# Kernel optimization log

Hardware: AMD Instinct MI355X
Metric: run time of the kernel (lower is better)

The kernel has to match this reference:

```python
import jax, jax.numpy as jnp
import numpy as np

N_NODES = 100000
N_EDGES = 1600000
D_IN = 128
HIDDEN = 128
N_CLASS = 10
N_LAYERS = 3


def setup_inputs() -> dict:
    key = jax.random.key(0)
    ks = jax.random.split(key, 12)
    x = jax.random.normal(ks[0], (N_NODES, D_IN), dtype=jnp.float32)
    edge_index = jax.random.randint(ks[1], (2, N_EDGES), 0, N_NODES, dtype=jnp.int64)
    edge_weight = jax.random.uniform(ks[2], (N_EDGES,), dtype=jnp.float32)
    # Per-layer GIN MLP params. D_IN == HIDDEN so all 3 layers stack cleanly.
    s = 1.0 / np.sqrt(HIDDEN)
    Wa = jax.random.uniform(ks[3], (N_LAYERS, HIDDEN, HIDDEN), minval=-s, maxval=s, dtype=jnp.float32)
    ba = jax.random.uniform(ks[4], (N_LAYERS, HIDDEN), minval=-s, maxval=s, dtype=jnp.float32)
    Wb = jax.random.uniform(ks[5], (N_LAYERS, HIDDEN, HIDDEN), minval=-s, maxval=s, dtype=jnp.float32)
    bb = jax.random.uniform(ks[6], (N_LAYERS, HIDDEN), minval=-s, maxval=s, dtype=jnp.float32)
    fcW = jax.random.uniform(ks[7], (HIDDEN, N_CLASS), minval=-s, maxval=s, dtype=jnp.float32)
    fcb = jax.random.uniform(ks[8], (N_CLASS,), minval=-s, maxval=s, dtype=jnp.float32)
    return {"x": x, "edge_index": edge_index, "edge_weight": edge_weight,
            "Wa": Wa, "ba": ba, "Wb": Wb, "bb": bb, "fcW": fcW, "fcb": fcb}


def reference(x, edge_index, edge_weight, Wa, ba, Wb, bb, fcW, fcb):
    # NOTE: edge_weight is loaded in the original forward but never used
    # (GINConv is invoked with only (x, edge_index)); we faithfully ignore it.
    src = edge_index[0]
    dst = edge_index[1]
    h = x
    for i in range(N_LAYERS):
        # GIN aggregation: (1 + eps) * h + sum_{j in N(i)} h_j, with eps = 0
        agg = jax.ops.segment_sum(h[src], dst, num_segments=N_NODES)  # [N, H]
        z = h + agg
        # 2-layer MLP: Linear -> ELU -> Linear -> ELU
        z = jax.nn.elu(z @ Wa[i] + ba[i])
        h = jax.nn.elu(z @ Wb[i] + bb[i])
    return h @ fcW + fcb  # [N, n_class]
```

## Files before the change

kernel.cpp:

```cpp
#include <hip/hip_runtime.h>
#include <hip/hip_bf16.h>
#include <math.h>

#define N_NODES 100000
#define N_PAD 100032
#define N_EDGES 1600000
#define HID 128
#define N_CLASS 10

#define NR2 256
#define RANGE2 391
#define PCAP2 8192
#define P_BLOCKS 512
#define P_SLICE (N_EDGES / P_BLOCKS)

typedef float f32x4 __attribute__((ext_vector_type(4)));
typedef short short8 __attribute__((ext_vector_type(8)));
typedef unsigned short us4 __attribute__((ext_vector_type(4)));

__device__ __forceinline__ unsigned short f2bf(float x) {
    unsigned u = __float_as_uint(x);
    unsigned r = u + 0x7FFF + ((u >> 16) & 1);
    return (unsigned short)(r >> 16);
}
__device__ __forceinline__ float bf2f(unsigned short h) {
    return __uint_as_float(((unsigned)h) << 16);
}
__device__ __forceinline__ float elu(float x) {
    return x > 0.f ? x : (expf(x) - 1.f);
}
__device__ __forceinline__ float4 us4f(us4 v) {
    float4 o;
    o.x = bf2f(v.x); o.y = bf2f(v.y); o.z = bf2f(v.z); o.w = bf2f(v.w);
    return o;
}


__global__ __launch_bounds__(256) void part_k(const int* __restrict__ src,
                                              const int* __restrict__ dst,
                                              int* __restrict__ gcnt,
                                              unsigned* __restrict__ gbuf) {
    __shared__ unsigned stash[P_SLICE];
    __shared__ unsigned char rbuf[P_SLICE];
    __shared__ int hist[NR2], cur[NR2], base[NR2];
    hist[threadIdx.x] = 0;
    cur[threadIdx.x] = 0;
    __syncthreads();
    const int e0 = blockIdx.x * P_SLICE;
    for (int i = threadIdx.x; i < P_SLICE; i += 256) {
        unsigned s = (unsigned)src[e0 + i];
        unsigned d = (unsigned)dst[e0 + i];
        unsigned r = d / RANGE2;
        unsigned dloc = d - r * RANGE2;
        stash[i] = s | (dloc << 17);
        rbuf[i] = (unsigned char)r;
        atomicAdd(&hist[r], 1);
    }
    __syncthreads();
    base[threadIdx.x] = atomicAdd(&gcnt[threadIdx.x], hist[threadIdx.x]);
    __syncthreads();
    for (int i = threadIdx.x; i < P_SLICE; i += 256) {
        unsigned r = rbuf[i];
        int off = atomicAdd(&cur[r], 1);
        int pos = base[r] + off;
        if (pos < PCAP2) gbuf[(size_t)r * PCAP2 + pos] = stash[i];
    }
}

__global__ void scanc_k(const int* __restrict__ gcnt, int* __restrict__ colbase,
                        int* __restrict__ row_ptr) {
    __shared__ int sh[NR2];
    int v = gcnt[threadIdx.x];
    sh[threadIdx.x] = v;
    __syncthreads();
    for (int off = 1; off < NR2; off <<= 1) {
        int t = (threadIdx.x >= off) ? sh[threadIdx.x - off] : 0;
        __syncthreads();
        sh[threadIdx.x] += t;
        __syncthreads();
    }
    colbase[threadIdx.x] = sh[threadIdx.x] - v;
    if (threadIdx.x == 0) row_ptr[N_NODES] = N_EDGES;
}

__global__ __launch_bounds__(256) void csort_k(const unsigned* __restrict__ gbuf,
                                               const int* __restrict__ gcnt,
                                               const int* __restrict__ colbase,
                                               int* __restrict__ row_ptr,
                                               int* __restrict__ col) {
    __shared__ int sorted[PCAP2];
    __shared__ int hist[512];
    __shared__ int cnt[512];
    __shared__ int run[400];
    const int q = blockIdx.x;
    const int tid = threadIdx.x;
    const int n2 = gcnt[q];
    const int cb = colbase[q];
    const int node0 = q * RANGE2;
    const unsigned* buf = gbuf + (size_t)q * PCAP2;

    hist[tid] = 0; hist[tid + 256] = 0;
    __syncthreads();
    for (int i = tid; i < n2; i += 256)
        atomicAdd(&hist[buf[i] >> 17], 1);
    __syncthreads();
    cnt[tid] = hist[tid];
    cnt[tid + 256] = hist[tid + 256];
    __syncthreads();
    for (int off = 1; off < 512; off <<= 1) {
        int v0 = (tid >= off) ? hist[tid - off] : 0;
        int v1 = hist[tid + 256 - off];
        __syncthreads();
        hist[tid] += v0;
        hist[tid + 256] += v1;
        __syncthreads();
    }
#pragma unroll
    for (int b = 0; b < 2; b++) {
        int i = tid + 256 * b;
        if (i < RANGE2) {
            int excl = hist[i] - cnt[i];
            run[i] = excl;
            int node = node0 + i;
            if (node < N_NODES) row_ptr[node] = cb + excl;
        }
    }
    __syncthreads();
    for (int i = tid; i < n2; i += 256) {
        unsigned w = buf[i];
        int pos = atomicAdd(&run[w >> 17], 1);
        sorted[pos] = (int)(w & 0x1FFFF);
    }
    __syncthreads();
    for (int i = tid; i < n2; i += 256) col[cb + i] = sorted[i];
}

__global__ __launch_bounds__(256) void cast_k(const float* __restrict__ x,
                                              unsigned short* __restrict__ hb) {
    int i = blockIdx.x * blockDim.x + threadIdx.x;
    if (i < N_NODES * (HID / 4)) {
        float4 v = ((const float4*)x)[i];
        us4 o = {f2bf(v.x), f2bf(v.y), f2bf(v.z), f2bf(v.w)};
        ((us4*)hb)[i] = o;
    }
}

__global__ void wsplit_k(const float* __restrict__ Wa, const float* __restrict__ Wb,
                         unsigned short* __restrict__ Whp) {
    int f = blockIdx.x * blockDim.x + threadIdx.x;
    if (f >= 6 * 16384) return;
    int g = f >> 14;
    int r = f & 16383;
    int j = r & 7;
    int L = (r >> 3) & 63;
    int t = r >> 9;
    int kb = t >> 3, nt = t & 7;
    int k = kb * 32 + ((L >> 4) & 3) * 8 + j;
    int n = nt * 16 + (L & 15);
    int layer = g >> 1;
    const float* W = (g & 1) ? Wb : Wa;
    Whp[f] = f2bf(W[layer * 16384 + k * 128 + n]);
}

__global__ void fcsplit_k(const float* __restrict__ fcW,
                          unsigned short* __restrict__ fcWph) {
    int f = blockIdx.x * blockDim.x + threadIdx.x;
    if (f >= 2048) return;
    int j = f & 7;
    int L = (f >> 3) & 63;
    int kb = f >> 9;
    int k = kb * 32 + ((L >> 4) & 3) * 8 + j;
    int n = L & 15;
    fcWph[f] = f2bf((n < N_CLASS) ? fcW[k * N_CLASS + n] : 0.f);
}

__global__ __launch_bounds__(256) void agg_k(const unsigned short* __restrict__ h,
                                             const int* __restrict__ row_ptr,
                                             const int* __restrict__ col,
                                             float* __restrict__ z) {
    const int half = (blockIdx.x * blockDim.x + threadIdx.x) >> 5;
    const int lane = threadIdx.x & 31;
    const int halfbase = threadIdx.x & 32;
    if (half >= N_NODES) return;
    const us4* hp = (const us4*)h;
    float4 acc = us4f(hp[(size_t)half * 32 + lane]);
    const int beg = row_ptr[half];
    const int end = row_ptr[half + 1];

    for (int base = beg; base < end; base += 32) {
        const int n = min(32, end - base);
        int myidx = (lane < n) ? col[base + lane] : 0;
        int j = 0;
        for (; j + 4 <= n; j += 4) {
            int i0 = __shfl(myidx, halfbase + j + 0, 64);
            int i1 = __shfl(myidx, halfbase + j + 1, 64);
            int i2 = __shfl(myidx, halfbase + j + 2, 64);
            int i3 = __shfl(myidx, halfbase + j + 3, 64);
            float4 v0 = us4f(hp[(size_t)i0 * 32 + lane]);
            float4 v1 = us4f(hp[(size_t)i1 * 32 + lane]);
            float4 v2 = us4f(hp[(size_t)i2 * 32 + lane]);
            float4 v3 = us4f(hp[(size_t)i3 * 32 + lane]);
            acc.x += v0.x; acc.y += v0.y; acc.z += v0.z; acc.w += v0.w;
            acc.x += v1.x; acc.y += v1.y; acc.z += v1.z; acc.w += v1.w;
            acc.x += v2.x; acc.y += v2.y; acc.z += v2.z; acc.w += v2.w;
            acc.x += v3.x; acc.y += v3.y; acc.z += v3.z; acc.w += v3.w;
        }
        for (; j < n; j++) {
            int i0 = __shfl(myidx, halfbase + j, 64);
            float4 v0 = us4f(hp[(size_t)i0 * 32 + lane]);
            acc.x += v0.x; acc.y += v0.y; acc.z += v0.z; acc.w += v0.w;
        }
    }
    ((float4*)z)[(size_t)half * 32 + lane] = acc;
}

__device__ __forceinline__ void gemm_phase(
    const unsigned short* Aph_,
    const unsigned short* __restrict__ Whi_g,
    const float* __restrict__ bias, int tid, f32x4 acc[2][4]) {
    const int L = tid & 63;
    const int w = tid >> 6;
    const int mt0 = (w >> 1) * 2;
    const int nt0 = (w & 1) * 4;
    const int lan15 = L & 15;
#pragma unroll
    for (int n = 0; n < 4; n++) {
        float b = bias[(nt0 + n) * 16 + lan15];
        f32x4 bv = {b, b, b, b};
        acc[0][n] = bv;
        acc[1][n] = bv;
    }
#pragma unroll
    for (int kb = 0; kb < 4; kb++) {
        short8 ah0 = *(const short8*)&Aph_[(((mt0 + 0) * 4 + kb) * 64 + L) * 8];
        short8 ah1 = *(const short8*)&Aph_[(((mt0 + 1) * 4 + kb) * 64 + L) * 8];
#pragma unroll
        for (int n = 0; n < 4; n++) {
            int widx = ((kb * 8 + nt0 + n) * 64 + L) * 8;
            short8 bh = *(const short8*)&Whi_g[widx];
            acc[0][n] = __builtin_amdgcn_mfma_f32_16x16x32_bf16(ah0, bh, acc[0][n], 0, 0, 0);
            acc[1][n] = __builtin_amdgcn_mfma_f32_16x16x32_bf16(ah1, bh, acc[1][n], 0, 0, 0);
        }
    }
}

template <int FC>
__device__ __forceinline__ void mlp_body(
    const float* __restrict__ zin,
    const unsigned short* __restrict__ Wahp,
    const unsigned short* __restrict__ Wbhp,
    const float* __restrict__ ba, const float* __restrict__ bb,
    unsigned short* __restrict__ hout,
    const unsigned short* __restrict__ fcWph,
    const float* __restrict__ fcb, float* __restrict__ out) {
    __shared__ unsigned short Aph[8192];

    const int tid = threadIdx.x;
    const int L = tid & 63;
    const int w = tid >> 6;
    const int mt0 = (w >> 1) * 2;
    const int nt0 = (w & 1) * 4;
    const int lan15 = L & 15;
    const int quad = L >> 4;
    const size_t node_base = (size_t)blockIdx.x * 64;

    {
        const float4* zin4 = (const float4*)(zin + node_base * HID);
#pragma unroll
        for (int r = 0; r < 8; r++) {
            int f = tid + 256 * r;
            int m = f >> 5;
            int k0 = (f & 31) * 4;
            float4 zv = zin4[f];
            int kb = k0 >> 5;
            int q = (k0 & 31) >> 3;
            int j0 = k0 & 7;
            int idx = (((m >> 4) * 4 + kb) * 64 + ((m & 15) + 16 * q)) * 8 + j0;
            us4 h4 = {f2bf(zv.x), f2bf(zv.y), f2bf(zv.z), f2bf(zv.w)};
            *(us4*)&Aph[idx] = h4;
        }
    }
    __syncthreads();

    {
        f32x4 acc[2][4];
        gemm_phase(Aph, Wahp, ba, tid, acc);
        __syncthreads();
#pragma unroll
        for (int i = 0; i < 2; i++) {
#pragma unroll
            for (int n = 0; n < 4; n++) {
                int kdim = (nt0 + n) * 16 + lan15;
                int kb2 = kdim >> 5;
                int q2 = (kdim & 31) >> 3;
                int j2 = kdim & 7;
#pragma unroll
                for (int r = 0; r < 4; r++) {
                    float v = elu(acc[i][n][r]);
                    int mrow = quad * 4 + r;
                    int idx = (((mt0 + i) * 4 + kb2) * 64 + (mrow + 16 * q2)) * 8 + j2;
                    Aph[idx] = f2bf(v);
                }
            }
        }
    }
    __syncthreads();

    {
        f32x4 acc[2][4];
        gemm_phase(Aph, Wbhp, bb, tid, acc);
        if (FC == 0) {
#pragma unroll
            for (int i = 0; i < 2; i++) {
#pragma unroll
                for (int n = 0; n < 4; n++) {
                    int ncol = (nt0 + n) * 16 + lan15;
#pragma unroll
                    for (int r = 0; r < 4; r++) {
                        int mrow = (mt0 + i) * 16 + quad * 4 + r;
                        hout[(node_base + mrow) * HID + ncol] = f2bf(elu(acc[i][n][r]));
                    }
                }
            }
        } else {
            __syncthreads();
#pragma unroll
            for (int i = 0; i < 2; i++) {
#pragma unroll
                for (int n = 0; n < 4; n++) {
                    int kdim = (nt0 + n) * 16 + lan15;
                    int kb2 = kdim >> 5;
                    int q2 = (kdim & 31) >> 3;
                    int j2 = kdim & 7;
#pragma unroll
                    for (int r = 0; r < 4; r++) {
                        float v = elu(acc[i][n][r]);
                        int mrow = quad * 4 + r;
                        int idx = (((mt0 + i) * 4 + kb2) * 64 + (mrow + 16 * q2)) * 8 + j2;
                        Aph[idx] = f2bf(v);
                    }
                }
            }
            __syncthreads();
            if ((w & 1) == 0) {
#pragma unroll
                for (int i = 0; i < 2; i++) {
                    int mt = mt0 + i;
                    float b = (lan15 < N_CLASS) ? fcb[lan15] : 0.f;
                    f32x4 acc2 = {b, b, b, b};
#pragma unroll
                    for (int kb = 0; kb < 4; kb++) {
                        short8 a = *(const short8*)&Aph[((mt * 4 + kb) * 64 + L) * 8];
                        short8 bh = *(const short8*)&fcWph[(kb * 64 + L) * 8];
                        acc2 = __builtin_amdgcn_mfma_f32_16x16x32_bf16(a, bh, acc2, 0, 0, 0);
                    }
#pragma unroll
                    for (int r = 0; r < 4; r++) {
                        size_t node = node_base + mt * 16 + quad * 4 + r;
                        if (node < N_NODES && lan15 < N_CLASS)
                            out[node * N_CLASS + lan15] = acc2[r];
                    }
                }
            }
        }
    }
}

__global__ __launch_bounds__(256) void mlp2_k(
    const float* __restrict__ zin,
    const unsigned short* __restrict__ Wahp,
    const unsigned short* __restrict__ Wbhp,
    const float* __restrict__ ba, const float* __restrict__ bb,
    unsigned short* __restrict__ hout) {
    mlp_body<0>(zin, Wahp, Wbhp, ba, bb, hout, nullptr, nullptr, nullptr);
}

__global__ __launch_bounds__(256) void mlp3_k(
    const float* __restrict__ zin,
    const unsigned short* __restrict__ Wahp,
    const unsigned short* __restrict__ Wbhp,
    const float* __restrict__ ba, const float* __restrict__ bb,
    const unsigned short* __restrict__ fcWph,
    const float* __restrict__ fcb, float* __restrict__ out) {
    mlp_body<1>(zin, Wahp, Wbhp, ba, bb, nullptr, fcWph, fcb, out);
}


extern "C" void kernel_launch(void* const* d_in, const int* in_sizes, int n_in,
                              void* d_out, int out_size, void* d_ws, size_t ws_size,
                              hipStream_t stream) {
    const float* x = (const float*)d_in[0];
    const int* ei = (const int*)d_in[1];
    const float* Wa = (const float*)d_in[3];
    const float* ba = (const float*)d_in[4];
    const float* Wb = (const float*)d_in[5];
    const float* bb = (const float*)d_in[6];
    const float* fcW = (const float*)d_in[7];
    const float* fcb = (const float*)d_in[8];
    float* out = (float*)d_out;

    const int* src = ei;
    const int* dst = ei + N_EDGES;

    char* w = (char*)d_ws;
    float* zbuf = (float*)w;          w += (size_t)N_PAD * HID * 4;
    unsigned short* hb = (unsigned short*)w; w += (size_t)N_PAD * HID * 2;
    int* row_ptr = (int*)w;  w += ((size_t)N_NODES + 8) * 4;
    int* gcnt = (int*)w;     w += NR2 * 4;
    int* colbase = (int*)w;  w += NR2 * 4;
    int* col = (int*)w;      w += (size_t)N_EDGES * 4;
    unsigned short* Whp = (unsigned short*)w; w += 6 * 16384 * 2;
    unsigned short* fcWph = (unsigned short*)w; w += 2048 * 2;
    unsigned* gbuf = (unsigned*)w; w += (size_t)NR2 * PCAP2 * 4;

    wsplit_k<<<(6 * 16384 + 255) / 256, 256, 0, stream>>>(Wa, Wb, Whp);
    fcsplit_k<<<8, 256, 0, stream>>>(fcW, fcWph);
    cast_k<<<(N_NODES * (HID / 4) + 255) / 256, 256, 0, stream>>>(x, hb);

    hipMemsetAsync(gcnt, 0, NR2 * 4, stream);
    part_k<<<P_BLOCKS, 256, 0, stream>>>(src, dst, gcnt, gbuf);
    scanc_k<<<1, 256, 0, stream>>>(gcnt, colbase, row_ptr);
    csort_k<<<NR2, 256, 0, stream>>>(gbuf, gcnt, colbase, row_ptr, col);

    const int AGG_BLOCKS = (N_NODES * 32 + 255) / 256;
    const int MLP_BLOCKS = (N_NODES + 63) / 64;

    agg_k<<<AGG_BLOCKS, 256, 0, stream>>>(hb, row_ptr, col, zbuf);
    mlp2_k<<<MLP_BLOCKS, 256, 0, stream>>>(zbuf, Whp, Whp + 16384, ba, bb, hb);
    agg_k<<<AGG_BLOCKS, 256, 0, stream>>>(hb, row_ptr, col, zbuf);
    mlp2_k<<<MLP_BLOCKS, 256, 0, stream>>>(zbuf, Whp + 2 * 16384, Whp + 3 * 16384,
                                           ba + 128, bb + 128, hb);
    agg_k<<<AGG_BLOCKS, 256, 0, stream>>>(hb, row_ptr, col, zbuf);
    mlp3_k<<<MLP_BLOCKS, 256, 0, stream>>>(zbuf, Whp + 4 * 16384, Whp + 5 * 16384,
                                           ba + 256, bb + 256,
                                           fcWph, fcb, out);
}
```

Measured before the change: 419.4 us.

## Fuse setup kernels, fold column scan into csort, store aggregates as bf16

Merges the partition, cast, weight-split and fc-split kernels into one multi-role setup kernel. The column-base scan moves into each csort block, which removes two launches. The aggregation output is now written as bf16 instead of fp32, and the first MLP GEMM reads A fragments directly from global memory instead of staging through LDS. Together these cut launch count and halve the z-buffer traffic, at the cost of rounding the aggregated sums to bf16 and doing uncoalesced per-lane global A loads.

```diff
diff --git a/kernel.cpp b/kernel.cpp
--- a/kernel.cpp
+++ b/kernel.cpp
@@ -13,6 +13,9 @@
 #define PCAP2 8192
 #define P_BLOCKS 512
 #define P_SLICE (N_EDGES / P_BLOCKS)
+#define CAST_ITEMS (N_NODES * (HID / 4))
+#define CAST_BLOCKS ((CAST_ITEMS + 2047) / 2048)
+#define WSPLIT_BLOCKS 384
 
 typedef float f32x4 __attribute__((ext_vector_type(4)));
 typedef short short8 __attribute__((ext_vector_type(8)));
@@ -35,67 +38,104 @@
     return o;
 }
 
-
-__global__ __launch_bounds__(256) void part_k(const int* __restrict__ src,
-                                              const int* __restrict__ dst,
-                                              int* __restrict__ gcnt,
-                                              unsigned* __restrict__ gbuf) {
+__global__ __launch_bounds__(256) void setup_k(
+    const int* __restrict__ src, const int* __restrict__ dst,
+    int* __restrict__ gcnt, unsigned* __restrict__ gbuf,
+    const float* __restrict__ x, unsigned short* __restrict__ hb,
+    const float* __restrict__ Wa, const float* __restrict__ Wb,
+    unsigned short* __restrict__ Whp,
+    const float* __restrict__ fcW, unsigned short* __restrict__ fcWph,
+    int* __restrict__ row_ptr) {
     __shared__ unsigned stash[P_SLICE];
     __shared__ unsigned char rbuf[P_SLICE];
     __shared__ int hist[NR2], cur[NR2], base[NR2];
-    hist[threadIdx.x] = 0;
-    cur[threadIdx.x] = 0;
-    __syncthreads();
-    const int e0 = blockIdx.x * P_SLICE;
-    for (int i = threadIdx.x; i < P_SLICE; i += 256) {
-        unsigned s = (unsigned)src[e0 + i];
-        unsigned d = (unsigned)dst[e0 + i];
-        unsigned r = d / RANGE2;
-        unsigned dloc = d - r * RANGE2;
-        stash[i] = s | (dloc << 17);
-        rbuf[i] = (unsigned char)r;
-        atomicAdd(&hist[r], 1);
-    }
-    __syncthreads();
-    base[threadIdx.x] = atomicAdd(&gcnt[threadIdx.x], hist[threadIdx.x]);
-    __syncthreads();
-    for (int i = threadIdx.x; i < P_SLICE; i += 256) {
-        unsigned r = rbuf[i];
-        int off = atomicAdd(&cur[r], 1);
-        int pos = base[r] + off;
-        if (pos < PCAP2) gbuf[(size_t)r * PCAP2 + pos] = stash[i];
-    }
-}
-
-__global__ void scanc_k(const int* __restrict__ gcnt, int* __restrict__ colbase,
-                        int* __restrict__ row_ptr) {
-    __shared__ int sh[NR2];
-    int v = gcnt[threadIdx.x];
-    sh[threadIdx.x] = v;
-    __syncthreads();
-    for (int off = 1; off < NR2; off <<= 1) {
-        int t = (threadIdx.x >= off) ? sh[threadIdx.x - off] : 0;
-        __syncthreads();
-        sh[threadIdx.x] += t;
-        __syncthreads();
-    }
-    colbase[threadIdx.x] = sh[threadIdx.x] - v;
-    if (threadIdx.x == 0) row_ptr[N_NODES] = N_EDGES;
+    const int b = blockIdx.x;
+    const int tid = threadIdx.x;
+
+    if (b < P_BLOCKS) {
+        hist[tid] = 0;
+        cur[tid] = 0;
+        __syncthreads();
+        const int e0 = b * P_SLICE;
+        for (int i = tid; i < P_SLICE; i += 256) {
+            unsigned s = (unsigned)src[e0 + i];
+            unsigned d = (unsigned)dst[e0 + i];
+            unsigned r = d / RANGE2;
+            unsigned dloc = d - r * RANGE2;
+            stash[i] = s | (dloc << 17);
+            rbuf[i] = (unsigned char)r;
+            atomicAdd(&hist[r], 1);
+        }
+        __syncthreads();
+        base[tid] = atomicAdd(&gcnt[tid], hist[tid]);
+        __syncthreads();
+        for (int i = tid; i < P_SLICE; i += 256) {
+            unsigned r = rbuf[i];
+            int off = atomicAdd(&cur[r], 1);
+            int pos = base[r] + off;
+            if (pos < PCAP2) gbuf[(size_t)r * PCAP2 + pos] = stash[i];
+        }
+    } else if (b < P_BLOCKS + CAST_BLOCKS) {
+        const int cb = b - P_BLOCKS;
+#pragma unroll
+        for (int it = 0; it < 8; it++) {
+            int i = cb * 2048 + it * 256 + tid;
+            if (i < CAST_ITEMS) {
+                float4 v = ((const float4*)x)[i];
+                us4 o = {f2bf(v.x), f2bf(v.y), f2bf(v.z), f2bf(v.w)};
+                ((us4*)hb)[i] = o;
+            }
+        }
+    } else if (b < P_BLOCKS + CAST_BLOCKS + WSPLIT_BLOCKS) {
+        int f = (b - P_BLOCKS - CAST_BLOCKS) * 256 + tid;
+        int g = f >> 14;
+        int r = f & 16383;
+        int j = r & 7;
+        int L = (r >> 3) & 63;
+        int t = r >> 9;
+        int kb = t >> 3, nt = t & 7;
+        int k = kb * 32 + ((L >> 4) & 3) * 8 + j;
+        int n = nt * 16 + (L & 15);
+        int layer = g >> 1;
+        const float* W = (g & 1) ? Wb : Wa;
+        Whp[f] = f2bf(W[layer * 16384 + k * 128 + n]);
+    } else {
+#pragma unroll
+        for (int it = 0; it < 8; it++) {
+            int f = it * 256 + tid;
+            int j = f & 7;
+            int L = (f >> 3) & 63;
+            int kb = f >> 9;
+            int k = kb * 32 + ((L >> 4) & 3) * 8 + j;
+            int n = L & 15;
+            fcWph[f] = f2bf((n < N_CLASS) ? fcW[k * N_CLASS + n] : 0.f);
+        }
+        if (tid == 0) row_ptr[N_NODES] = N_EDGES;
+    }
 }
 
 __global__ __launch_bounds__(256) void csort_k(const unsigned* __restrict__ gbuf,
                                                const int* __restrict__ gcnt,
-                                               const int* __restrict__ colbase,
                                                int* __restrict__ row_ptr,
                                                int* __restrict__ col) {
     __shared__ int sorted[PCAP2];
     __shared__ int hist[512];
     __shared__ int cnt[512];
     __shared__ int run[400];
+    __shared__ int gsc[NR2];
     const int q = blockIdx.x;
     const int tid = threadIdx.x;
+
+    gsc[tid] = gcnt[tid];
+    __syncthreads();
+    for (int off = 1; off < NR2; off <<= 1) {
+        int t = (tid >= off) ? gsc[tid - off] : 0;
+        __syncthreads();
+        gsc[tid] += t;
+        __syncthreads();
+    }
+    const int cb = (q > 0) ? gsc[q - 1] : 0;
     const int n2 = gcnt[q];
-    const int cb = colbase[q];
     const int node0 = q * RANGE2;
     const unsigned* buf = gbuf + (size_t)q * PCAP2;
 
@@ -116,8 +156,8 @@
         __syncthreads();
     }
 #pragma unroll
-    for (int b = 0; b < 2; b++) {
-        int i = tid + 256 * b;
+    for (int bb = 0; bb < 2; bb++) {
+        int i = tid + 256 * bb;
         if (i < RANGE2) {
             int excl = hist[i] - cnt[i];
             run[i] = excl;
@@ -135,49 +175,10 @@
     for (int i = tid; i < n2; i += 256) col[cb + i] = sorted[i];
 }
 
-__global__ __launch_bounds__(256) void cast_k(const float* __restrict__ x,
-                                              unsigned short* __restrict__ hb) {
-    int i = blockIdx.x * blockDim.x + threadIdx.x;
-    if (i < N_NODES * (HID / 4)) {
-        float4 v = ((const float4*)x)[i];
-        us4 o = {f2bf(v.x), f2bf(v.y), f2bf(v.z), f2bf(v.w)};
-        ((us4*)hb)[i] = o;
-    }
-}
-
-__global__ void wsplit_k(const float* __restrict__ Wa, const float* __restrict__ Wb,
-                         unsigned short* __restrict__ Whp) {
-    int f = blockIdx.x * blockDim.x + threadIdx.x;
-    if (f >= 6 * 16384) return;
-    int g = f >> 14;
-    int r = f & 16383;
-    int j = r & 7;
-    int L = (r >> 3) & 63;
-    int t = r >> 9;
-    int kb = t >> 3, nt = t & 7;
-    int k = kb * 32 + ((L >> 4) & 3) * 8 + j;
-    int n = nt * 16 + (L & 15);
-    int layer = g >> 1;
-    const float* W = (g & 1) ? Wb : Wa;
-    Whp[f] = f2bf(W[layer * 16384 + k * 128 + n]);
-}
-
-__global__ void fcsplit_k(const float* __restrict__ fcW,
-                          unsigned short* __restrict__ fcWph) {
-    int f = blockIdx.x * blockDim.x + threadIdx.x;
-    if (f >= 2048) return;
-    int j = f & 7;
-    int L = (f >> 3) & 63;
-    int kb = f >> 9;
-    int k = kb * 32 + ((L >> 4) & 3) * 8 + j;
-    int n = L & 15;
-    fcWph[f] = f2bf((n < N_CLASS) ? fcW[k * N_CLASS + n] : 0.f);
-}
-
 __global__ __launch_bounds__(256) void agg_k(const unsigned short* __restrict__ h,
                                              const int* __restrict__ row_ptr,
                                              const int* __restrict__ col,
-                                             float* __restrict__ z) {
+                                             unsigned short* __restrict__ z) {
     const int half = (blockIdx.x * blockDim.x + threadIdx.x) >> 5;
     const int lane = threadIdx.x & 31;
     const int halfbase = threadIdx.x & 32;
@@ -211,10 +212,43 @@
             acc.x += v0.x; acc.y += v0.y; acc.z += v0.z; acc.w += v0.w;
         }
     }
-    ((float4*)z)[(size_t)half * 32 + lane] = acc;
-}
-
-__device__ __forceinline__ void gemm_phase(
+    us4 o = {f2bf(acc.x), f2bf(acc.y), f2bf(acc.z), f2bf(acc.w)};
+    ((us4*)z)[(size_t)half * 32 + lane] = o;
+}
+
+__device__ __forceinline__ void gemm1_g(
+    const unsigned short* __restrict__ zrow,
+    const unsigned short* __restrict__ Whi_g,
+    const float* __restrict__ bias, int tid, f32x4 acc[2][4]) {
+    const int L = tid & 63;
+    const int w = tid >> 6;
+    const int mt0 = (w >> 1) * 2;
+    const int nt0 = (w & 1) * 4;
+    const int lan15 = L & 15;
+    const int quad = L >> 4;
+#pragma unroll
+    for (int n = 0; n < 4; n++) {
+        float b = bias[(nt0 + n) * 16 + lan15];
+        f32x4 bv = {b, b, b, b};
+        acc[0][n] = bv;
+        acc[1][n] = bv;
+    }
+    const unsigned short* rowA0 = zrow + (mt0 * 16 + lan15) * HID + quad * 8;
+    const unsigned short* rowA1 = rowA0 + 16 * HID;
+#pragma unroll
+    for (int kb = 0; kb < 4; kb++) {
+        short8 ah0 = *(const short8*)&rowA0[kb * 32];
+        short8 ah1 = *(const short8*)&rowA1[kb * 32];
+#pragma unroll
+        for (int n = 0; n < 4; n++) {
+            short8 bh = *(const short8*)&Whi_g[((kb * 8 + nt0 + n) * 64 + L) * 8];
+            acc[0][n] = __builtin_amdgcn_mfma_f32_16x16x32_bf16(ah0, bh, acc[0][n], 0, 0, 0);
+            acc[1][n] = __builtin_amdgcn_mfma_f32_16x16x32_bf16(ah1, bh, acc[1][n], 0, 0, 0);
+        }
+    }
+}
+
+__device__ __forceinline__ void gemm_lds(
     const unsigned short* Aph_,
     const unsigned short* __restrict__ Whi_g,
     const float* __restrict__ bias, int tid, f32x4 acc[2][4]) {
@@ -236,8 +270,7 @@
         short8 ah1 = *(const short8*)&Aph_[(((mt0 + 1) * 4 + kb) * 64 + L) * 8];
 #pragma unroll
         for (int n = 0; n < 4; n++) {
-            int widx = ((kb * 8 + nt0 + n) * 64 + L) * 8;
-            short8 bh = *(const short8*)&Whi_g[widx];
+            short8 bh = *(const short8*)&Whi_g[((kb * 8 + nt0 + n) * 64 + L) * 8];
             acc[0][n] = __builtin_amdgcn_mfma_f32_16x16x32_bf16(ah0, bh, acc[0][n], 0, 0, 0);
             acc[1][n] = __builtin_amdgcn_mfma_f32_16x16x32_bf16(ah1, bh, acc[1][n], 0, 0, 0);
         }
@@ -246,7 +279,7 @@
 
 template <int FC>
 __device__ __forceinline__ void mlp_body(
-    const float* __restrict__ zin,
+    const unsigned short* __restrict__ zb,
     const unsigned short* __restrict__ Wahp,
     const unsigned short* __restrict__ Wbhp,
     const float* __restrict__ ba, const float* __restrict__ bb,
@@ -265,27 +298,8 @@
     const size_t node_base = (size_t)blockIdx.x * 64;
 
     {
-        const float4* zin4 = (const float4*)(zin + node_base * HID);
-#pragma unroll
-        for (int r = 0; r < 8; r++) {
-            int f = tid + 256 * r;
-            int m = f >> 5;
-            int k0 = (f & 31) * 4;
-            float4 zv = zin4[f];
-            int kb = k0 >> 5;
-            int q = (k0 & 31) >> 3;
-            int j0 = k0 & 7;
-            int idx = (((m >> 4) * 4 + kb) * 64 + ((m & 15) + 16 * q)) * 8 + j0;
-            us4 h4 = {f2bf(zv.x), f2bf(zv.y), f2bf(zv.z), f2bf(zv.w)};
-            *(us4*)&Aph[idx] = h4;
-        }
-    }
-    __syncthreads();
-
-    {
         f32x4 acc[2][4];
-        gemm_phase(Aph, Wahp, ba, tid, acc);
-        __syncthreads();
+        gemm1_g(zb + node_base * HID, Wahp, ba, tid, acc);
 #pragma unroll
         for (int i = 0; i < 2; i++) {
 #pragma unroll
@@ -308,7 +322,7 @@
 
     {
         f32x4 acc[2][4];
-        gemm_phase(Aph, Wbhp, bb, tid, acc);
+        gemm_lds(Aph, Wbhp, bb, tid, acc);
         if (FC == 0) {
 #pragma unroll
             for (int i = 0; i < 2; i++) {
@@ -367,22 +381,22 @@
 }
 
 __global__ __launch_bounds__(256) void mlp2_k(
-    const float* __restrict__ zin,
+    const unsigned short* __restrict__ zb,
     const unsigned short* __restrict__ Wahp,
     const unsigned short* __restrict__ Wbhp,
     const float* __restrict__ ba, const float* __restrict__ bb,
     unsigned short* __restrict__ hout) {
-    mlp_body<0>(zin, Wahp, Wbhp, ba, bb, hout, nullptr, nullptr, nullptr);
+    mlp_body<0>(zb, Wahp, Wbhp, ba, bb, hout, nullptr, nullptr, nullptr);
 }
 
 __global__ __launch_bounds__(256) void mlp3_k(
-    const float* __restrict__ zin,
+    const unsigned short* __restrict__ zb,
     const unsigned short* __restrict__ Wahp,
     const unsigned short* __restrict__ Wbhp,
     const float* __restrict__ ba, const float* __restrict__ bb,
     const unsigned short* __restrict__ fcWph,
     const float* __restrict__ fcb, float* __restrict__ out) {
-    mlp_body<1>(zin, Wahp, Wbhp, ba, bb, nullptr, fcWph, fcb, out);
+    mlp_body<1>(zb, Wahp, Wbhp, ba, bb, nullptr, fcWph, fcb, out);
 }
 
 
@@ -403,35 +417,31 @@
     const int* dst = ei + N_EDGES;
 
     char* w = (char*)d_ws;
-    float* zbuf = (float*)w;          w += (size_t)N_PAD * HID * 4;
+    unsigned short* zb = (unsigned short*)w; w += (size_t)N_PAD * HID * 2;
     unsigned short* hb = (unsigned short*)w; w += (size_t)N_PAD * HID * 2;
     int* row_ptr = (int*)w;  w += ((size_t)N_NODES + 8) * 4;
     int* gcnt = (int*)w;     w += NR2 * 4;
-    int* colbase = (int*)w;  w += NR2 * 4;
     int* col = (int*)w;      w += (size_t)N_EDGES * 4;
     unsigned short* Whp = (unsigned short*)w; w += 6 * 16384 * 2;
     unsigned short* fcWph = (unsigned short*)w; w += 2048 * 2;
     unsigned* gbuf = (unsigned*)w; w += (size_t)NR2 * PCAP2 * 4;
 
-    wsplit_k<<<(6 * 16384 + 255) / 256, 256, 0, stream>>>(Wa, Wb, Whp);
-    fcsplit_k<<<8, 256, 0, stream>>>(fcW, fcWph);
-    cast_k<<<(N_NODES * (HID / 4) + 255) / 256, 256, 0, stream>>>(x, hb);
-
     hipMemsetAsync(gcnt, 0, NR2 * 4, stream);
-    part_k<<<P_BLOCKS, 256, 0, stream>>>(src, dst, gcnt, gbuf);
-    scanc_k<<<1, 256, 0, stream>>>(gcnt, colbase, row_ptr);
-    csort_k<<<NR2, 256, 0, stream>>>(gbuf, gcnt, colbase, row_ptr, col);
+    const int SETUP_BLOCKS = P_BLOCKS + CAST_BLOCKS + WSPLIT_BLOCKS + 1;
+    setup_k<<<SETUP_BLOCKS, 256, 0, stream>>>(src, dst, gcnt, gbuf, x, hb,
+                                              Wa, Wb, Whp, fcW, fcWph, row_ptr);
+    csort_k<<<NR2, 256, 0, stream>>>(gbuf, gcnt, row_ptr, col);
 
     const int AGG_BLOCKS = (N_NODES * 32 + 255) / 256;
     const int MLP_BLOCKS = (N_NODES + 63) / 64;
 
-    agg_k<<<AGG_BLOCKS, 256, 0, stream>>>(hb, row_ptr, col, zbuf);
-    mlp2_k<<<MLP_BLOCKS, 256, 0, stream>>>(zbuf, Whp, Whp + 16384, ba, bb, hb);
-    agg_k<<<AGG_BLOCKS, 256, 0, stream>>>(hb, row_ptr, col, zbuf);
-    mlp2_k<<<MLP_BLOCKS, 256, 0, stream>>>(zbuf, Whp + 2 * 16384, Whp + 3 * 16384,
+    agg_k<<<AGG_BLOCKS, 256, 0, stream>>>(hb, row_ptr, col, zb);
+    mlp2_k<<<MLP_BLOCKS, 256, 0, stream>>>(zb, Whp, Whp + 16384, ba, bb, hb);
+    agg_k<<<AGG_BLOCKS, 256, 0, stream>>>(hb, row_ptr, col, zb);
+    mlp2_k<<<MLP_BLOCKS, 256, 0, stream>>>(zb, Whp + 2 * 16384, Whp + 3 * 16384,
                                            ba + 128, bb + 128, hb);
-    agg_k<<<AGG_BLOCKS, 256, 0, stream>>>(hb, row_ptr, col, zbuf);
-    mlp3_k<<<MLP_BLOCKS, 256, 0, stream>>>(zbuf, Whp + 4 * 16384, Whp + 5 * 16384,
+    agg_k<<<AGG_BLOCKS, 256, 0, stream>>>(hb, row_ptr, col, zb);
+    mlp3_k<<<MLP_BLOCKS, 256, 0, stream>>>(zb, Whp + 4 * 16384, Whp + 5 * 16384,
                                            ba + 256, bb + 256,
                                            fcWph, fcb, out);
 }
```

Measured after the change: 402.5 us. 1.04x faster.
